# Kernel optimization log

Hardware: AMD Instinct MI355X
Metric: run time of the kernel (lower is better)

## Reference

```python
import jax, jax.numpy as jnp
import numpy as np

D_MODEL = 768
D_STATE = 16
D_CONV = 4
EXPAND = 2
INNER = EXPAND * D_MODEL  # 1536
BATCH = 2
SEQLEN = 2048


def setup_inputs() -> dict:
    key = jax.random.key(0)
    ks = jax.random.split(key, 8)
    s = 0.02
    return {
        "hidden_states": jax.random.normal(ks[0], (BATCH, SEQLEN, D_MODEL), jnp.float32),
        "in_proj_w": jax.random.normal(ks[1], (2 * INNER, D_MODEL), jnp.float32) * (D_MODEL ** -0.5),
        "out_proj_w": jax.random.normal(ks[2], (D_MODEL, INNER), jnp.float32) * (INNER ** -0.5),
        "dt_proj_w": jax.random.normal(ks[3], (INNER, INNER), jnp.float32) * (INNER ** -0.5),
        "dt_proj_b": jnp.zeros((INNER,), jnp.float32),
        "conv_w": jax.random.normal(ks[4], (INNER, D_CONV), jnp.float32) * s,
        "conv_b": jnp.zeros((INNER,), jnp.float32),
        "A_log": jnp.zeros((INNER, D_STATE), jnp.float32),
        "B_param": jax.random.normal(ks[5], (INNER, D_STATE), jnp.float32) * s,
        "C_param": jax.random.normal(ks[6], (INNER, D_STATE), jnp.float32) * s,
        "D_param": jnp.ones((INNER,), jnp.float32),
        "dt_bias": jnp.zeros((INNER,), jnp.float32),
    }


def reference(hidden_states, in_proj_w, out_proj_w, dt_proj_w, dt_proj_b,
              conv_w, conv_b, A_log, B_param, C_param, D_param, dt_bias):
    # in_proj: (B, L, d_model) -> (B, L, 2*inner); split into projected / gate
    xz = jnp.einsum('bld,od->blo', hidden_states, in_proj_w)
    proj, gate = jnp.split(xz, 2, axis=-1)
    x = jnp.transpose(proj, (0, 2, 1))  # (B, inner, L) channel-first

    # depthwise causal conv (left-pad d_conv-1) + bias + SiLU
    conv = jax.lax.conv_general_dilated(
        x, conv_w[:, None, :], window_strides=(1,),
        padding=[(D_CONV - 1, 0)], feature_group_count=INNER,
        dimension_numbers=('NCH', 'OIH', 'NCH'))
    u = jax.nn.silu(conv + conv_b[None, :, None])  # (B, inner, L)

    # dt projection (1x1 linear on channel-first) + softplus(dt + dt_bias)
    delta = jnp.einsum('oc,bcl->bol', dt_proj_w, u) + dt_proj_b[None, :, None]
    dt = jax.nn.softplus(delta + dt_bias[None, :, None])  # (B, inner, L)

    A = -jnp.exp(A_log)  # (inner, d_state)
    # discretize: dA = exp(dt * A), dBu = dt * u * B   -> (B, inner, L, N)
    dA = jnp.exp(dt[..., None] * A[None, :, None, :])
    dBu = (dt * u)[..., None] * B_param[None, :, None, :]

    dA_t = jnp.moveaxis(dA, 2, 0)    # (L, B, inner, N)
    dBu_t = jnp.moveaxis(dBu, 2, 0)  # (L, B, inner, N)

    def step(h, inp):
        a_t, b_t = inp
        h = a_t * h + b_t                      # (B, inner, N)
        y = jnp.einsum('bdn,dn->bd', h, C_param)
        return h, y

    h0 = jnp.zeros(dA_t.shape[1:], dA.dtype)
    _, ys = jax.lax.scan(step, h0, (dA_t, dBu_t))  # ys: (L, B, inner)
    y = jnp.transpose(ys, (1, 2, 0))               # (B, inner, L)

    z = jnp.transpose(gate, (0, 2, 1))             # (B, inner, L)
    y = (y + D_param[None, :, None] * u) * jax.nn.silu(z)

    # out_proj: (B, inner, L) -> (B, L, d_model)
    return jnp.einsum('bdl,od->blo', y, out_proj_w)
```

## Files before the change

### kernel.cpp

```cpp
#include <hip/hip_runtime.h>
#include <cstdint>
#include <cstddef>

#define D_MODEL 768
#define D_STATE 16
#define D_CONV  4
#define INNER   1536
#define BATCH   2
#define SEQLEN  2048
#define M_TOK   (BATCH * SEQLEN)
#define NCH     (BATCH * INNER)
#define NCHUNK  64
#define CL      (SEQLEN / NCHUNK)

typedef unsigned short u16;
typedef __attribute__((ext_vector_type(4))) unsigned short us4;
typedef __attribute__((ext_vector_type(8))) short bf8;
typedef __attribute__((ext_vector_type(4))) float f32x4;

__device__ __forceinline__ u16 f2bf(float f) {
    uint32_t x = __float_as_uint(f);
    return (u16)((x + 0x7fffu + ((x >> 16) & 1u)) >> 16);
}
__device__ __forceinline__ float bf2f(u16 h) {
    return __uint_as_float(((uint32_t)h) << 16);
}

__global__ __launch_bounds__(256) void cvt_hilo4(
    const float* __restrict__ s0, u16* __restrict__ h0, u16* __restrict__ l0, int n0,
    const float* __restrict__ s1, u16* __restrict__ h1, u16* __restrict__ l1, int n1,
    const float* __restrict__ s2, u16* __restrict__ h2, u16* __restrict__ l2, int n2,
    const float* __restrict__ s3, u16* __restrict__ h3, u16* __restrict__ l3, int n3)
{
    int j = blockIdx.x * 256 + threadIdx.x;
    const float* s; u16* hh; u16* ll;
    if (j < n0) { s = s0; hh = h0; ll = l0; }
    else {
        j -= n0;
        if (j < n1) { s = s1; hh = h1; ll = l1; }
        else {
            j -= n1;
            if (j < n2) { s = s2; hh = h2; ll = l2; }
            else {
                j -= n2;
                if (j >= n3) return;
                s = s3; hh = h3; ll = l3;
            }
        }
    }
    const float4 v = ((const float4*)s)[j];
    us4 h, l;
    h.x = f2bf(v.x); l.x = f2bf(v.x - bf2f(h.x));
    h.y = f2bf(v.y); l.y = f2bf(v.y - bf2f(h.y));
    h.z = f2bf(v.z); l.z = f2bf(v.z - bf2f(h.z));
    h.w = f2bf(v.w); l.w = f2bf(v.w - bf2f(h.w));
    ((us4*)hh)[j] = h;
    ((us4*)ll)[j] = l;
}

template <int MODE, int FRM, int FRN>
__global__ __launch_bounds__(256) void gemm_mfma(
    const u16* __restrict__ Ah_g, const u16* __restrict__ Al_g,
    const u16* __restrict__ Bh_g, const u16* __restrict__ Bl_g,
    float* __restrict__ C, const float* __restrict__ bias1,
    const float* __restrict__ bias2, int M, int N, int K)
{
    constexpr int BM = FRM * 32;
    constexpr int BN = FRN * 32;
    constexpr int SBUF = (BM + BN) * 128;
    __shared__ __align__(16) char smem[2 * SBUF];

    const int tid = threadIdx.x;
    const int w = tid >> 6;
    const int lane = tid & 63;

    const int gx = gridDim.x;
    const int nwg = gx * gridDim.y;
    int f = blockIdx.y * gx + blockIdx.x;
    f = (f & 7) * (nwg >> 3) + (f >> 3);
    const int bm = (f / gx) * BM;
    const int bn = (f % gx) * BN;

    const int wm = (w >> 1) * (FRM * 16);
    const int wn = (w & 1) * (FRN * 16);

    const int g8 = lane & 7;
    const int r8 = lane >> 3;
    const int src = g8 ^ r8;
    const int scol = (src & 3) * 8;
    const bool use_lo = (src & 4) != 0;

    const u16* pA[FRM];
    const u16* pB[FRN];
#pragma unroll
    for (int c = 0; c < FRM; ++c) {
        const int row = w * (FRM * 8) + c * 8 + r8;
        pA[c] = (use_lo ? Al_g : Ah_g) + (size_t)(bm + row) * K + scol;
    }
#pragma unroll
    for (int c = 0; c < FRN; ++c) {
        const int row = w * (FRN * 8) + c * 8 + r8;
        pB[c] = (use_lo ? Bl_g : Bh_g) + (size_t)(bn + row) * K + scol;
    }

    f32x4 acc[FRM][FRN] = {};
    const int fr = lane & 15;
    const int gk = lane >> 4;
    const int ghi = gk ^ (fr & 7);

    const int nt = K >> 5;

#define STAGE_ALL(pp, kt)                                                           \
    {                                                                               \
        char* sb = smem + (pp) * SBUF;                                              \
        _Pragma("unroll")                                                           \
        for (int c = 0; c < FRM; ++c)                                               \
            __builtin_amdgcn_global_load_lds(                                       \
                (const __attribute__((address_space(1))) void*)(pA[c] + (kt)),      \
                (__attribute__((address_space(3))) void*)(sb + (w * FRM + c) * 1024), \
                16, 0, 0);                                                          \
        _Pragma("unroll")                                                           \
        for (int c = 0; c < FRN; ++c)                                               \
            __builtin_amdgcn_global_load_lds(                                       \
                (const __attribute__((address_space(1))) void*)(pB[c] + (kt)),      \
                (__attribute__((address_space(3))) void*)(sb + BM * 128 + (w * FRN + c) * 1024), \
                16, 0, 0);                                                          \
    }

    STAGE_ALL(0, 0)

    int p = 0;
    for (int t = 0; t < nt; ++t) {
        if (t + 1 < nt) {
            STAGE_ALL(p ^ 1, (t + 1) * 32)
            if constexpr (FRM + FRN == 8) {
                asm volatile("s_waitcnt vmcnt(8)" ::: "memory");
            } else if constexpr (FRM + FRN == 6) {
                asm volatile("s_waitcnt vmcnt(6)" ::: "memory");
            } else {
                asm volatile("s_waitcnt vmcnt(4)" ::: "memory");
            }
        } else {
            asm volatile("s_waitcnt vmcnt(0)" ::: "memory");
        }
        __builtin_amdgcn_s_barrier();
        __builtin_amdgcn_sched_barrier(0);
        __builtin_amdgcn_s_setprio(1);

        const char* A0 = smem + p * SBUF;
        const char* B0 = A0 + BM * 128;
        bf8 ah[FRM], al[FRM], bh[FRN], bl[FRN];
#pragma unroll
        for (int i = 0; i < FRM; ++i) {
            const int row = wm + i * 16 + fr;
            ah[i] = *(const bf8*)(A0 + row * 128 + ghi * 16);
            al[i] = *(const bf8*)(A0 + row * 128 + (ghi ^ 4) * 16);
        }
#pragma unroll
        for (int j = 0; j < FRN; ++j) {
            const int row = wn + j * 16 + fr;
            bh[j] = *(const bf8*)(B0 + row * 128 + ghi * 16);
            bl[j] = *(const bf8*)(B0 + row * 128 + (ghi ^ 4) * 16);
        }
#pragma unroll
        for (int i = 0; i < FRM; ++i)
#pragma unroll
            for (int j = 0; j < FRN; ++j) {
                acc[i][j] = __builtin_amdgcn_mfma_f32_16x16x32_bf16(ah[i], bh[j], acc[i][j], 0, 0, 0);
                acc[i][j] = __builtin_amdgcn_mfma_f32_16x16x32_bf16(ah[i], bl[j], acc[i][j], 0, 0, 0);
                acc[i][j] = __builtin_amdgcn_mfma_f32_16x16x32_bf16(al[i], bh[j], acc[i][j], 0, 0, 0);
            }

        __builtin_amdgcn_s_setprio(0);
        __builtin_amdgcn_sched_barrier(0);
        __builtin_amdgcn_s_barrier();
        p ^= 1;
    }
#undef STAGE_ALL

    const int r0 = (lane >> 4) * 4;
#pragma unroll
    for (int i = 0; i < FRM; ++i) {
        const int row0 = bm + wm + i * 16 + r0;
#pragma unroll
        for (int j = 0; j < FRN; ++j) {
            const int col = bn + wn + j * 16 + fr;
            float add = 0.f;
            if constexpr (MODE == 1) add = bias1[col] + bias2[col];
#pragma unroll
            for (int r = 0; r < 4; ++r) {
                float v = acc[i][j][r];
                if constexpr (MODE == 1) {
                    const float xx = v + add;
                    v = (xx > 20.f) ? xx : log1pf(expf(xx));
                }
                C[(size_t)(row0 + r) * N + col] = v;
            }
        }
    }
}

__global__ __launch_bounds__(256) void conv_silu_kernel(
    const float* __restrict__ xz, const float* __restrict__ cw,
    const float* __restrict__ cb, u16* __restrict__ uh, u16* __restrict__ ul)
{
    const int idx = blockIdx.x * 256 + threadIdx.x;
    const int c4 = (idx % (INNER / 4)) * 4;
    const int m  = idx / (INNER / 4);
    if (m >= M_TOK) return;
    const int b = m >> 11;
    const int l = m & (SEQLEN - 1);

    float wt[4][4];
#pragma unroll
    for (int i = 0; i < 4; ++i) {
        const float4 wv = *(const float4*)&cw[(c4 + i) * 4];
        wt[i][0] = wv.x; wt[i][1] = wv.y; wt[i][2] = wv.z; wt[i][3] = wv.w;
    }
    const float4 bias = *(const float4*)&cb[c4];
    float a[4] = {bias.x, bias.y, bias.z, bias.w};

#pragma unroll
    for (int j = 0; j < 4; ++j) {
        const int ll = l - 3 + j;
        if (ll >= 0) {
            const float4 x = *(const float4*)&xz[(size_t)(b * SEQLEN + ll) * (2 * INNER) + c4];
            a[0] = fmaf(x.x, wt[0][j], a[0]);
            a[1] = fmaf(x.y, wt[1][j], a[1]);
            a[2] = fmaf(x.z, wt[2][j], a[2]);
            a[3] = fmaf(x.w, wt[3][j], a[3]);
        }
    }
    float o[4];
#pragma unroll
    for (int i = 0; i < 4; ++i) o[i] = a[i] / (1.f + __expf(-a[i]));

    us4 h, lo;
    h.x = f2bf(o[0]); lo.x = f2bf(o[0] - bf2f(h.x));
    h.y = f2bf(o[1]); lo.y = f2bf(o[1] - bf2f(h.y));
    h.z = f2bf(o[2]); lo.z = f2bf(o[2] - bf2f(h.z));
    h.w = f2bf(o[3]); lo.w = f2bf(o[3] - bf2f(h.w));
    const size_t vi = ((size_t)m * INNER + c4) / 4;
    ((us4*)uh)[vi] = h;
    ((us4*)ul)[vi] = lo;
}

__global__ __launch_bounds__(256) void scan_pass1(
    const float* __restrict__ dt, const u16* __restrict__ uh,
    const u16* __restrict__ ul, const float* __restrict__ A_log,
    const float* __restrict__ Bp, float* __restrict__ hend,
    float* __restrict__ Sdt)
{
    const int ch = blockIdx.x * 256 + threadIdx.x;
    const int c = blockIdx.y;
    const int b = (ch >= INNER) ? 1 : 0;
    const int d = ch - b * INNER;

    float A2[D_STATE], Bn[D_STATE];
#pragma unroll
    for (int n = 0; n < D_STATE; n += 4) {
        const float4 av = *(const float4*)&A_log[d * D_STATE + n];
        const float4 bv = *(const float4*)&Bp[d * D_STATE + n];
        A2[n+0] = -expf(av.x) * 1.44269504f; Bn[n+0] = bv.x;
        A2[n+1] = -expf(av.y) * 1.44269504f; Bn[n+1] = bv.y;
        A2[n+2] = -expf(av.z) * 1.44269504f; Bn[n+2] = bv.z;
        A2[n+3] = -expf(av.w) * 1.44269504f; Bn[n+3] = bv.w;
    }

    const size_t base = (size_t)(b * SEQLEN + c * CL) * INNER + d;
    const float* dtp = dt + base;
    const u16* uhp = uh + base;
    const u16* ulp = ul + base;

    float h[D_STATE] = {};
    float S = 0.f;

    float dtv = dtp[0];
    float uv = bf2f(uhp[0]) + bf2f(ulp[0]);

    for (int l = 0; l < CL; ++l) {
        float dtn = 0.f, un = 0.f;
        if (l + 1 < CL) {
            dtn = dtp[(size_t)(l + 1) * INNER];
            un = bf2f(uhp[(size_t)(l + 1) * INNER]) + bf2f(ulp[(size_t)(l + 1) * INNER]);
        }
        const float dtu = dtv * uv;
        S += dtv;
#pragma unroll
        for (int n = 0; n < D_STATE; ++n) {
            const float dA = exp2f(dtv * A2[n]);
            h[n] = fmaf(dA, h[n], dtu * Bn[n]);
        }
        dtv = dtn; uv = un;
    }

#pragma unroll
    for (int n = 0; n < D_STATE; ++n)
        hend[((size_t)c * D_STATE + n) * NCH + ch] = h[n];
    Sdt[(size_t)c * NCH + ch] = S;
}

__global__ __launch_bounds__(256) void scan_combine(
    const float* __restrict__ hend, const float* __restrict__ Sdt,
    const float* __restrict__ A_log, float* __restrict__ h0all)
{
    const int idx = blockIdx.x * 256 + threadIdx.x;
    const int n = idx / NCH;
    const int ch = idx - n * NCH;
    const int b = (ch >= INNER) ? 1 : 0;
    const int d = ch - b * INNER;
    const float A2 = -expf(A_log[d * D_STATE + n]) * 1.44269504f;

    float h0 = 0.f;
    for (int c = 0; c < NCHUNK; ++c) {
        const size_t o = ((size_t)c * D_STATE + n) * NCH + ch;
        h0all[o] = h0;
        const float P = exp2f(A2 * Sdt[(size_t)c * NCH + ch]);
        h0 = fmaf(P, h0, hend[o]);
    }
}

__global__ __launch_bounds__(256) void scan_pass2(
    const float* __restrict__ dt, const u16* __restrict__ uh,
    const u16* __restrict__ ul, const float* __restrict__ xz,
    const float* __restrict__ A_log, const float* __restrict__ Bp,
    const float* __restrict__ Cp, const float* __restrict__ Dp,
    const float* __restrict__ h0all, u16* __restrict__ ygh,
    u16* __restrict__ ygl)
{
    const int ch = blockIdx.x * 256 + threadIdx.x;
    const int c = blockIdx.y;
    const int b = (ch >= INNER) ? 1 : 0;
    const int d = ch - b * INNER;

    float A2[D_STATE], Bn[D_STATE], Cn[D_STATE];
#pragma unroll
    for (int n = 0; n < D_STATE; n += 4) {
        const float4 av = *(const float4*)&A_log[d * D_STATE + n];
        const float4 bv = *(const float4*)&Bp[d * D_STATE + n];
        const float4 cv = *(const float4*)&Cp[d * D_STATE + n];
        A2[n+0] = -expf(av.x) * 1.44269504f; Bn[n+0] = bv.x; Cn[n+0] = cv.x;
        A2[n+1] = -expf(av.y) * 1.44269504f; Bn[n+1] = bv.y; Cn[n+1] = cv.y;
        A2[n+2] = -expf(av.z) * 1.44269504f; Bn[n+2] = bv.z; Cn[n+2] = cv.z;
        A2[n+3] = -expf(av.w) * 1.44269504f; Bn[n+3] = bv.w; Cn[n+3] = cv.w;
    }
    const float Dd = Dp[d];

    float h[D_STATE];
#pragma unroll
    for (int n = 0; n < D_STATE; ++n)
        h[n] = h0all[((size_t)c * D_STATE + n) * NCH + ch];

    const size_t base = (size_t)(b * SEQLEN + c * CL) * INNER + d;
    const float* dtp = dt + base;
    const u16* uhp = uh + base;
    const u16* ulp = ul + base;
    const float* zp = xz + (size_t)(b * SEQLEN + c * CL) * (2 * INNER) + INNER + d;
    u16* yhp = ygh + base;
    u16* ylp = ygl + base;

    float dtv = dtp[0];
    float uv = bf2f(uhp[0]) + bf2f(ulp[0]);
    float zv = zp[0];

    for (int l = 0; l < CL; ++l) {
        float dtn = 0.f, un = 0.f, zn = 0.f;
        if (l + 1 < CL) {
            dtn = dtp[(size_t)(l + 1) * INNER];
            un = bf2f(uhp[(size_t)(l + 1) * INNER]) + bf2f(ulp[(size_t)(l + 1) * INNER]);
            zn = zp[(size_t)(l + 1) * (2 * INNER)];
        }
        const float dtu = dtv * uv;
        float y = 0.f;
#pragma unroll
        for (int n = 0; n < D_STATE; ++n) {
            const float dA = exp2f(dtv * A2[n]);
            h[n] = fmaf(dA, h[n], dtu * Bn[n]);
            y = fmaf(h[n], Cn[n], y);
        }
        const float sig = 1.f / (1.f + __expf(-zv));
        const float val = (y + Dd * uv) * (zv * sig);
        const u16 hv = f2bf(val);
        yhp[(size_t)l * INNER] = hv;
        ylp[(size_t)l * INNER] = f2bf(val - bf2f(hv));
        dtv = dtn; uv = un; zv = zn;
    }
}

extern "C" void kernel_launch(void* const* d_in, const int* in_sizes, int n_in,
                              void* d_out, int out_size, void* d_ws, size_t ws_size,
                              hipStream_t stream)
{
    const float* hs      = (const float*)d_in[0];
    const float* in_w    = (const float*)d_in[1];
    const float* out_w   = (const float*)d_in[2];
    const float* dt_w    = (const float*)d_in[3];
    const float* dt_b    = (const float*)d_in[4];
    const float* conv_w  = (const float*)d_in[5];
    const float* conv_b  = (const float*)d_in[6];
    const float* A_log   = (const float*)d_in[7];
    const float* Bp      = (const float*)d_in[8];
    const float* Cp      = (const float*)d_in[9];
    const float* Dp      = (const float*)d_in[10];
    const float* dt_bias = (const float*)d_in[11];
    float* out = (float*)d_out;

    float* xz    = (float*)d_ws;
    float* dtf   = xz + (size_t)M_TOK * 2 * INNER;
    float* hend  = dtf + (size_t)M_TOK * INNER;
    float* Sdt   = hend + (size_t)NCHUNK * D_STATE * NCH;
    float* h0all = Sdt + (size_t)NCHUNK * NCH;
    u16* uh  = (u16*)(h0all + (size_t)NCHUNK * D_STATE * NCH);
    u16* ul  = uh  + (size_t)M_TOK * INNER;
    u16* hsh = ul  + (size_t)M_TOK * INNER;
    u16* hsl = hsh + (size_t)M_TOK * D_MODEL;
    u16* ygh = hsl + (size_t)M_TOK * D_MODEL;
    u16* ygl = ygh + (size_t)M_TOK * INNER;
    u16* iwh = ygl + (size_t)M_TOK * INNER;
    u16* iwl = iwh + (size_t)2 * INNER * D_MODEL;
    u16* dwh = iwl + (size_t)2 * INNER * D_MODEL;
    u16* dwl = dwh + (size_t)INNER * INNER;
    u16* owh = dwl + (size_t)INNER * INNER;
    u16* owl = owh + (size_t)D_MODEL * INNER;

    const dim3 blk(256);

    {
        const int n0 = M_TOK * D_MODEL / 4;
        const int n1 = 2 * INNER * D_MODEL / 4;
        const int n2 = INNER * INNER / 4;
        const int n3 = D_MODEL * INNER / 4;
        const int ntot = n0 + n1 + n2 + n3;
        cvt_hilo4<<<dim3((ntot + 255) / 256), blk, 0, stream>>>(
            hs, hsh, hsl, n0, in_w, iwh, iwl, n1,
            dt_w, dwh, dwl, n2, out_w, owh, owl, n3);
    }

    gemm_mfma<0, 4, 4><<<dim3(2 * INNER / 128, M_TOK / 128), blk, 0, stream>>>(
        hsh, hsl, iwh, iwl, xz, nullptr, nullptr, M_TOK, 2 * INNER, D_MODEL);

    conv_silu_kernel<<<dim3((M_TOK * (INNER / 4)) / 256), blk, 0, stream>>>(
        xz, conv_w, conv_b, uh, ul);

    gemm_mfma<1, 4, 2><<<dim3(INNER / 64, M_TOK / 128), blk, 0, stream>>>(
        uh, ul, dwh, dwl, dtf, dt_b, dt_bias, M_TOK, INNER, INNER);

    scan_pass1<<<dim3(NCH / 256, NCHUNK), blk, 0, stream>>>(
        dtf, uh, ul, A_log, Bp, hend, Sdt);
    scan_combine<<<dim3((D_STATE * NCH) / 256), blk, 0, stream>>>(
        hend, Sdt, A_log, h0all);
    scan_pass2<<<dim3(NCH / 256, NCHUNK), blk, 0, stream>>>(
        dtf, uh, ul, xz, A_log, Bp, Cp, Dp, h0all, ygh, ygl);

    gemm_mfma<0, 2, 2><<<dim3(D_MODEL / 64, M_TOK / 64), blk, 0, stream>>>(
        ygh, ygl, owh, owl, out, nullptr, nullptr, M_TOK, D_MODEL, INNER);
}
```

Baseline: 333.1 us.

## Load GEMM B operand straight to registers, bypassing LDS staging

The MFMA GEMM no longer stages the B tile (hi and lo bf16 parts) through shared memory. Each wave now loads its own B fragments from global memory directly into registers, one k-step ahead, issued right after the MFMA block. Only the A tile is still double-buffered in LDS via global_load_lds, which halves the LDS footprint and removes the B LDS reads. In exchange, waves that share the same N columns fetch duplicate B data through the cache, the per-lane global loads are less coalesced, and the hand-written vmcnt values now assume FRM is 2 or 4.

```diff
diff --git a/kernel.cpp b/kernel.cpp
--- a/kernel.cpp
+++ b/kernel.cpp
@@ -67,8 +67,8 @@
 {
     constexpr int BM = FRM * 32;
     constexpr int BN = FRN * 32;
-    constexpr int SBUF = (BM + BN) * 128;
-    __shared__ __align__(16) char smem[2 * SBUF];
+    constexpr int ABUF = BM * 128;
+    __shared__ __align__(16) char smem[2 * ABUF];
 
     const int tid = threadIdx.x;
     const int w = tid >> 6;
@@ -86,81 +86,72 @@
 
     const int g8 = lane & 7;
     const int r8 = lane >> 3;
-    const int src = g8 ^ r8;
-    const int scol = (src & 3) * 8;
-    const bool use_lo = (src & 4) != 0;
+    const int srcg = g8 ^ r8;
+    const int scol = (srcg & 3) * 8;
+    const bool use_lo = (srcg & 4) != 0;
 
     const u16* pA[FRM];
-    const u16* pB[FRN];
 #pragma unroll
     for (int c = 0; c < FRM; ++c) {
         const int row = w * (FRM * 8) + c * 8 + r8;
         pA[c] = (use_lo ? Al_g : Ah_g) + (size_t)(bm + row) * K + scol;
     }
-#pragma unroll
-    for (int c = 0; c < FRN; ++c) {
-        const int row = w * (FRN * 8) + c * 8 + r8;
-        pB[c] = (use_lo ? Bl_g : Bh_g) + (size_t)(bn + row) * K + scol;
-    }
-
-    f32x4 acc[FRM][FRN] = {};
+
     const int fr = lane & 15;
     const int gk = lane >> 4;
+    const u16* pBh[FRN];
+    const u16* pBl[FRN];
+#pragma unroll
+    for (int j = 0; j < FRN; ++j) {
+        const int row = bn + wn + j * 16 + fr;
+        pBh[j] = Bh_g + (size_t)row * K + gk * 8;
+        pBl[j] = Bl_g + (size_t)row * K + gk * 8;
+    }
+
+    f32x4 acc[FRM][FRN] = {};
     const int ghi = gk ^ (fr & 7);
 
     const int nt = K >> 5;
 
-#define STAGE_ALL(pp, kt)                                                           \
+#define STAGE_A(pp, kt)                                                             \
     {                                                                               \
-        char* sb = smem + (pp) * SBUF;                                              \
+        char* sb = smem + (pp) * ABUF;                                              \
         _Pragma("unroll")                                                           \
         for (int c = 0; c < FRM; ++c)                                               \
             __builtin_amdgcn_global_load_lds(                                       \
                 (const __attribute__((address_space(1))) void*)(pA[c] + (kt)),      \
                 (__attribute__((address_space(3))) void*)(sb + (w * FRM + c) * 1024), \
                 16, 0, 0);                                                          \
-        _Pragma("unroll")                                                           \
-        for (int c = 0; c < FRN; ++c)                                               \
-            __builtin_amdgcn_global_load_lds(                                       \
-                (const __attribute__((address_space(1))) void*)(pB[c] + (kt)),      \
-                (__attribute__((address_space(3))) void*)(sb + BM * 128 + (w * FRN + c) * 1024), \
-                16, 0, 0);                                                          \
-    }
-
-    STAGE_ALL(0, 0)
+    }
+
+    STAGE_A(0, 0)
+    bf8 bh[FRN], bl[FRN];
+#pragma unroll
+    for (int j = 0; j < FRN; ++j) {
+        bh[j] = *(const bf8*)(pBh[j]);
+        bl[j] = *(const bf8*)(pBl[j]);
+    }
 
     int p = 0;
     for (int t = 0; t < nt; ++t) {
-        if (t + 1 < nt) {
-            STAGE_ALL(p ^ 1, (t + 1) * 32)
-            if constexpr (FRM + FRN == 8) {
-                asm volatile("s_waitcnt vmcnt(8)" ::: "memory");
-            } else if constexpr (FRM + FRN == 6) {
-                asm volatile("s_waitcnt vmcnt(6)" ::: "memory");
-            } else {
-                asm volatile("s_waitcnt vmcnt(4)" ::: "memory");
-            }
+        const int kpre = (t + 1 < nt ? t + 1 : t) * 32;
+        STAGE_A(p ^ 1, kpre)
+        if constexpr (FRM == 4) {
+            asm volatile("s_waitcnt vmcnt(4)" ::: "memory");
         } else {
-            asm volatile("s_waitcnt vmcnt(0)" ::: "memory");
+            asm volatile("s_waitcnt vmcnt(2)" ::: "memory");
         }
         __builtin_amdgcn_s_barrier();
         __builtin_amdgcn_sched_barrier(0);
         __builtin_amdgcn_s_setprio(1);
 
-        const char* A0 = smem + p * SBUF;
-        const char* B0 = A0 + BM * 128;
-        bf8 ah[FRM], al[FRM], bh[FRN], bl[FRN];
+        const char* A0 = smem + p * ABUF;
+        bf8 ah[FRM], al[FRM];
 #pragma unroll
         for (int i = 0; i < FRM; ++i) {
             const int row = wm + i * 16 + fr;
             ah[i] = *(const bf8*)(A0 + row * 128 + ghi * 16);
             al[i] = *(const bf8*)(A0 + row * 128 + (ghi ^ 4) * 16);
-        }
-#pragma unroll
-        for (int j = 0; j < FRN; ++j) {
-            const int row = wn + j * 16 + fr;
-            bh[j] = *(const bf8*)(B0 + row * 128 + ghi * 16);
-            bl[j] = *(const bf8*)(B0 + row * 128 + (ghi ^ 4) * 16);
         }
 #pragma unroll
         for (int i = 0; i < FRM; ++i)
@@ -172,11 +163,16 @@
             }
 
         __builtin_amdgcn_s_setprio(0);
+#pragma unroll
+        for (int j = 0; j < FRN; ++j) {
+            bh[j] = *(const bf8*)(pBh[j] + kpre);
+            bl[j] = *(const bf8*)(pBl[j] + kpre);
+        }
         __builtin_amdgcn_sched_barrier(0);
         __builtin_amdgcn_s_barrier();
         p ^= 1;
     }
-#undef STAGE_ALL
+#undef STAGE_A
 
     const int r0 = (lane >> 4) * 4;
 #pragma unroll
```

After: 428.1 us. 28.5% more time.
